# Performance work log

Hardware: AMD Instinct MI355X
Metric: run time of the kernel (lower is better)

The kernel has to match this reference:

```python
import jax, jax.numpy as jnp
import numpy as np

B, S, D = 2, 2048, 4096
H, KVH, HD = 32, 8, 128          # n_heads, n_kv_heads, head_dim
N_REP = H // KVH                 # GQA repeat factor
ROPE_THETA = 10000.0
NEG = -1e9                       # finite stand-in for -inf additive mask


def setup_inputs() -> dict:
    key = jax.random.key(0)
    ks = jax.random.split(key, 5)
    x = jax.random.normal(ks[0], (B, S, D), jnp.float32)
    wq = jax.random.normal(ks[1], (D, H * HD), jnp.float32) * 0.02
    wk = jax.random.normal(ks[2], (D, KVH * HD), jnp.float32) * 0.02
    wv = jax.random.normal(ks[3], (D, KVH * HD), jnp.float32) * 0.02
    wo = jax.random.normal(ks[4], (D, D), jnp.float32) * 0.02
    # rotary frequencies: freq_cis[t, j] = exp(i * t * theta^(-2j/HD))
    inv_freq = 1.0 / (ROPE_THETA ** (jnp.arange(0, HD, 2, dtype=jnp.float32) / HD))
    angles = jnp.arange(S, dtype=jnp.float32)[:, None] * inv_freq[None, :]  # [S, HD/2]
    cos, sin = jnp.cos(angles), jnp.sin(angles)
    # causal additive mask [S, S]
    i = jnp.arange(S)
    mask = jnp.where(i[None, :] > i[:, None], NEG, 0.0).astype(jnp.float32)
    return {"x": x, "cos": cos, "sin": sin, "mask": mask,
            "wq": wq, "wk": wk, "wv": wv, "wo": wo, "start_pos": 0}


def _apply_rope(t, cos, sin):
    # t: [B, S, nH, HD] -> rotate consecutive pairs, matching view_as_complex semantics
    tp = t.reshape(*t.shape[:-1], HD // 2, 2)
    t0, t1 = tp[..., 0], tp[..., 1]
    c = cos[None, :, None, :]  # [1, S, 1, HD/2]
    s = sin[None, :, None, :]
    o0 = t0 * c - t1 * s
    o1 = t0 * s + t1 * c
    return jnp.stack([o0, o1], axis=-1).reshape(t.shape)


def reference(x, cos, sin, mask, wq, wk, wv, wo, start_pos):
    bs, seq_len, _ = x.shape
    q = (x @ wq).reshape(bs, seq_len, H, HD)
    k = (x @ wk).reshape(bs, seq_len, KVH, HD)
    v = (x @ wv).reshape(bs, seq_len, KVH, HD)
    q = _apply_rope(q, cos, sin)
    k = _apply_rope(k, cos, sin)
    # start_pos == 0 full prefill: KV cache slice [:, :start_pos+seq_len] == k, v
    # GQA: repeat_interleave kv heads (each kv head repeated N_REP times consecutively)
    k = jnp.repeat(k, N_REP, axis=2)  # [B, S, H, HD]
    v = jnp.repeat(v, N_REP, axis=2)
    attn = jnp.einsum('bqhd,bkhd->bhqk', q, k) / jnp.sqrt(jnp.float32(HD))
    attn = attn + mask[None, None, :, :]
    p = jax.nn.softmax(attn.astype(jnp.float32), axis=-1).astype(q.dtype)
    out = jnp.einsum('bhqk,bkhd->bqhd', p, v).reshape(bs, seq_len, D)
    return out @ wo
```

## Files before the change

kernel.cpp:

```cpp
#include <hip/hip_runtime.h>
#include <stdint.h>

typedef unsigned short u16;
typedef __attribute__((ext_vector_type(8))) short bf16x8;
typedef __attribute__((ext_vector_type(4))) float f32x4;

#if __has_builtin(__builtin_amdgcn_exp2f)
  #define ATTN_EXP(x) __builtin_amdgcn_exp2f(x)
  #define ATTN_QSC 0.12751746f
  #define ATTN_NOFF -11.5415603f
#else
  #define ATTN_EXP(x) __expf(x)
  #define ATTN_QSC 0.08838834764831845f
  #define ATTN_NOFF -8.0f
#endif

__device__ __forceinline__ u16 f2bf(float f) {
  uint32_t x = __float_as_uint(f);
  x += 0x7fffu + ((x >> 16) & 1u);
  return (u16)(x >> 16);
}
__device__ __forceinline__ float bf2f(u16 u) {
  return __uint_as_float(((uint32_t)u) << 16);
}
__device__ __forceinline__ void gload_lds16(const void* g, void* l) {
  __builtin_amdgcn_global_load_lds(
      (const __attribute__((address_space(1))) void*)g,
      (__attribute__((address_space(3))) void*)l, 16, 0, 0);
}

__device__ __forceinline__ float rope_rot(float a, int col, int srow,
                                          const float* __restrict__ cosT,
                                          const float* __restrict__ sinT) {
  float p = __shfl_xor(a, 1, 64);
  int d = (col & 127) >> 1;
  float c = cosT[srow * 64 + d];
  float sn = sinT[srow * 64 + d];
  return (col & 1) ? (p * sn + a * c) : (a * c - p * sn);
}

__global__ __launch_bounds__(256) void cvt_kernel(const float* __restrict__ x,
                                                  u16* __restrict__ y) {
  int i = blockIdx.x * 256 + threadIdx.x;
  float4 v = ((const float4*)x)[i];
  ushort4 o = make_ushort4(f2bf(v.x), f2bf(v.y), f2bf(v.z), f2bf(v.w));
  ((ushort4*)y)[i] = o;
}

__global__ __launch_bounds__(256) void transpose_cvt(const float* __restrict__ W,
                                                     u16* __restrict__ Wt,
                                                     int Kd, int Nd) {
  __shared__ float t[32][33];
  int k0 = blockIdx.y * 32, n0 = blockIdx.x * 32;
  int tx = threadIdx.x, ty = threadIdx.y;
  #pragma unroll
  for (int i = ty; i < 32; i += 8)
    t[i][tx] = W[(size_t)(k0 + i) * Nd + n0 + tx];
  __syncthreads();
  #pragma unroll
  for (int i = ty; i < 32; i += 8)
    Wt[(size_t)(n0 + i) * Kd + k0 + tx] = f2bf(t[tx][i]);
}

__global__ __launch_bounds__(256, 2) void gemm_kv(const u16* __restrict__ A,
                                                  const u16* __restrict__ Bt,
                                                  u16* __restrict__ Kout,
                                                  u16* __restrict__ Vt,
                                                  const float* __restrict__ cosT,
                                                  const float* __restrict__ sinT) {
  const int K = 4096;
  const int NK = 64;
  __shared__ __attribute__((aligned(16))) u16 sA[3][128 * 64];
  __shared__ __attribute__((aligned(16))) u16 sB[2][128 * 64];
  const int tid = threadIdx.x;
  const int wave = tid >> 6, lane = tid & 63;
  const int lr = lane & 15, lq = lane >> 4;
  int lin = blockIdx.y * gridDim.x + blockIdx.x;
  int cpx = (gridDim.x * gridDim.y) >> 3;
  int swz = (lin & 7) * cpx + (lin >> 3);
  const int bm = (swz >> 4) * 128, bn = (swz & 15) * 128;
  const int wm = (wave >> 1) * 64, wn = (wave & 1) * 64;

  f32x4 acc[4][4] = {};

  auto stageA = [&](int j) {
    u16* dst = &sA[j % 3][0];
    #pragma unroll
    for (int c = 0; c < 4; ++c) {
      int e = (c * 256 + tid) * 8;
      int r = e >> 6, col = e & 63;
      gload_lds16(A + (size_t)(bm + r) * K + j * 64 + (col ^ ((r & 7) << 3)), dst + e);
    }
  };
  auto stageB = [&](int j) {
    u16* dst = &sB[j & 1][0];
    #pragma unroll
    for (int c = 0; c < 4; ++c) {
      int e = (c * 256 + tid) * 8;
      int r = e >> 6, col = e & 63;
      gload_lds16(Bt + (size_t)(bn + r) * K + j * 64 + (col ^ ((r & 7) << 3)), dst + e);
    }
  };
  auto readA = [&](bf16x8* af, const u16* a_, int ks) {
    #pragma unroll
    for (int mf = 0; mf < 4; ++mf) {
      int row = wm + mf * 16 + lr;
      af[mf] = *(const bf16x8*)(a_ + row * 64 + ((ks * 32 + lq * 8) ^ ((row & 7) << 3)));
    }
  };
  auto readB = [&](bf16x8* bfv, const u16* b_, int ks) {
    #pragma unroll
    for (int nf = 0; nf < 4; ++nf) {
      int row = wn + nf * 16 + lr;
      bfv[nf] = *(const bf16x8*)(b_ + row * 64 + ((ks * 32 + lq * 8) ^ ((row & 7) << 3)));
    }
  };

  bf16x8 afP[4], bfP[4], afQ[4], bfQ[4];

  stageA(0); stageB(0); stageA(1); stageB(1);
  asm volatile("s_waitcnt vmcnt(8)" ::: "memory");
  asm volatile("s_barrier" ::: "memory");
  readA(afP, sA[0], 0); readB(bfP, sB[0], 0);

  for (int j = 0; j < NK; ++j) {
    const u16* a_ = sA[j % 3];
    const u16* b_ = sB[j & 1];
    const u16* an = sA[(j + 1) % 3];
    const u16* bn_ = sB[(j + 1) & 1];
    readA(afQ, a_, 1); readB(bfQ, b_, 1);
    if (j + 2 < NK) stageA(j + 2);
    asm volatile("s_waitcnt lgkmcnt(8)" ::: "memory");
    __builtin_amdgcn_sched_barrier(0);
    __builtin_amdgcn_s_setprio(1);
    #pragma unroll
    for (int mf = 0; mf < 4; ++mf)
      #pragma unroll
      for (int nf = 0; nf < 4; ++nf)
        acc[mf][nf] = __builtin_amdgcn_mfma_f32_16x16x32_bf16(afP[mf], bfP[nf],
                                                              acc[mf][nf], 0, 0, 0);
    __builtin_amdgcn_s_setprio(0);
    if (j + 2 < NK) asm volatile("s_waitcnt vmcnt(4)" ::: "memory");
    else            asm volatile("s_waitcnt vmcnt(0)" ::: "memory");
    asm volatile("s_barrier" ::: "memory");
    readA(afP, an, 0); readB(bfP, bn_, 0);
    if (j + 2 < NK) stageB(j + 2);
    asm volatile("s_waitcnt lgkmcnt(8)" ::: "memory");
    __builtin_amdgcn_sched_barrier(0);
    __builtin_amdgcn_s_setprio(1);
    #pragma unroll
    for (int mf = 0; mf < 4; ++mf)
      #pragma unroll
      for (int nf = 0; nf < 4; ++nf)
        acc[mf][nf] = __builtin_amdgcn_mfma_f32_16x16x32_bf16(afQ[mf], bfQ[nf],
                                                              acc[mf][nf], 0, 0, 0);
    __builtin_amdgcn_s_setprio(0);
  }

  #pragma unroll
  for (int i = 0; i < 4; ++i) {
    #pragma unroll
    for (int j = 0; j < 4; ++j) {
      int colg = bn + wn + j * 16 + lr;
      if (bn < 1024) {
        #pragma unroll
        for (int r = 0; r < 4; ++r) {
          int row = bm + wm + i * 16 + lq * 4 + r;
          float o = rope_rot(acc[i][j][r], colg, row & 2047, cosT, sinT);
          Kout[(size_t)row * 1024 + colg] = f2bf(o);
        }
      } else {
        int col = colg - 1024;
        int row0 = bm + wm + i * 16 + lq * 4;
        int bb = row0 >> 11, s = row0 & 2047;
        ushort4 pk = make_ushort4(f2bf(acc[i][j][0]), f2bf(acc[i][j][1]),
                                  f2bf(acc[i][j][2]), f2bf(acc[i][j][3]));
        *(ushort4*)(Vt + ((size_t)bb * 1024 + col) * 2048 + s) = pk;
      }
    }
  }
}

template <int EPI, bool ROPE>
__global__ __launch_bounds__(512, 2) void gemm256(const u16* __restrict__ A,
                                                  const u16* __restrict__ Bt,
                                                  void* __restrict__ Cout,
                                                  int M, int N, int K,
                                                  const float* __restrict__ cosT,
                                                  const float* __restrict__ sinT,
                                                  float post) {
  __shared__ __attribute__((aligned(16))) u16 sA[3][256 * 64];
  __shared__ __attribute__((aligned(16))) u16 sB[2][256 * 64];
  const int tid = threadIdx.x;
  const int wid = tid >> 6, lane = tid & 63;
  const int lr = lane & 15, lq = lane >> 4;
  const int nbn = N >> 8;
  int lin = blockIdx.y * gridDim.x + blockIdx.x;
  int cpx = (gridDim.x * gridDim.y) >> 3;
  int swz = (lin & 7) * cpx + (lin >> 3);
  const int bm = (swz / nbn) * 256, bn = (swz % nbn) * 256;
  const int wrow = (wid >> 2) * 128, wcol = (wid & 3) * 64;
  const int NK = K >> 6;

  f32x4 acc[8][4] = {};

  auto stageA = [&](int j) {
    u16* dst = &sA[j % 3][0];
    #pragma unroll
    for (int c = 0; c < 4; ++c) {
      int e = (c * 512 + tid) * 8;
      int r = e >> 6, col = e & 63;
      gload_lds16(A + (size_t)(bm + r) * K + j * 64 + (col ^ ((r & 7) << 3)), dst + e);
    }
  };
  auto stageB = [&](int j) {
    u16* dst = &sB[j & 1][0];
    #pragma unroll
    for (int c = 0; c < 4; ++c) {
      int e = (c * 512 + tid) * 8;
      int r = e >> 6, col = e & 63;
      gload_lds16(Bt + (size_t)(bn + r) * K + j * 64 + (col ^ ((r & 7) << 3)), dst + e);
    }
  };
  auto readA = [&](bf16x8* af, const u16* a_, int ks) {
    #pragma unroll
    for (int mf = 0; mf < 8; ++mf) {
      int row = wrow + mf * 16 + lr;
      af[mf] = *(const bf16x8*)(a_ + row * 64 + ((ks * 32 + lq * 8) ^ ((row & 7) << 3)));
    }
  };
  auto readB = [&](bf16x8* bfv, const u16* b_, int ks) {
    #pragma unroll
    for (int nf = 0; nf < 4; ++nf) {
      int row = wcol + nf * 16 + lr;
      bfv[nf] = *(const bf16x8*)(b_ + row * 64 + ((ks * 32 + lq * 8) ^ ((row & 7) << 3)));
    }
  };

  bf16x8 afP[8], bfP[4], afQ[8], bfQ[4];

  stageB(0); stageA(0); stageA(1); stageB(1);
  asm volatile("s_waitcnt vmcnt(8)" ::: "memory");
  asm volatile("s_barrier" ::: "memory");
  readA(afP, sA[0], 0); readB(bfP, sB[0], 0);

  for (int j = 0; j < NK; ++j) {
    const u16* a_ = sA[j % 3];
    const u16* b_ = sB[j & 1];
    const u16* an = sA[(j + 1) % 3];
    const u16* bn = sB[(j + 1) & 1];
    readA(afQ, a_, 1); readB(bfQ, b_, 1);
    if (j + 2 < NK) stageA(j + 2);
    asm volatile("s_waitcnt lgkmcnt(12)" ::: "memory");
    __builtin_amdgcn_sched_barrier(0);
    __builtin_amdgcn_s_setprio(1);
    #pragma unroll
    for (int mf = 0; mf < 8; ++mf)
      #pragma unroll
      for (int nf = 0; nf < 4; ++nf)
        acc[mf][nf] = __builtin_amdgcn_mfma_f32_16x16x32_bf16(afP[mf], bfP[nf],
                                                              acc[mf][nf], 0, 0, 0);
    __builtin_amdgcn_s_setprio(0);
    if (j + 2 < NK) asm volatile("s_waitcnt vmcnt(4)" ::: "memory");
    else            asm volatile("s_waitcnt vmcnt(0)" ::: "memory");
    asm volatile("s_barrier" ::: "memory");
    readA(afP, an, 0); readB(bfP, bn, 0);
    if (j + 2 < NK) stageB(j + 2);
    asm volatile("s_waitcnt lgkmcnt(12)" ::: "memory");
    __builtin_amdgcn_sched_barrier(0);
    __builtin_amdgcn_s_setprio(1);
    #pragma unroll
    for (int mf = 0; mf < 8; ++mf)
      #pragma unroll
      for (int nf = 0; nf < 4; ++nf)
        acc[mf][nf] = __builtin_amdgcn_mfma_f32_16x16x32_bf16(afQ[mf], bfQ[nf],
                                                              acc[mf][nf], 0, 0, 0);
    __builtin_amdgcn_s_setprio(0);
  }

  #pragma unroll
  for (int mf = 0; mf < 8; ++mf) {
    #pragma unroll
    for (int nf = 0; nf < 4; ++nf) {
      #pragma unroll
      for (int r = 0; r < 4; ++r) {
        int row = bm + wrow + mf * 16 + lq * 4 + r;
        int col = bn + wcol + nf * 16 + lr;
        if (ROPE) {
          float o = rope_rot(acc[mf][nf][r], col, row & 2047, cosT, sinT);
          ((u16*)Cout)[(size_t)row * N + col] = f2bf(o * post);
        } else if (EPI == 0) {
          ((u16*)Cout)[(size_t)row * N + col] = f2bf(acc[mf][nf][r]);
        } else {
          ((float*)Cout)[(size_t)row * N + col] = acc[mf][nf][r];
        }
      }
    }
  }
}

__global__ __launch_bounds__(256, 2) void attn_kernel(const u16* __restrict__ Q,
                                                      const u16* __restrict__ Kb,
                                                      const u16* __restrict__ Vt,
                                                      u16* __restrict__ O) {
  __shared__ __attribute__((aligned(16))) u16 sK[2][64 * 128];
  __shared__ __attribute__((aligned(16))) u16 sV[2][128 * 64];
  __shared__ __attribute__((aligned(16))) u16 sP[4][16 * 64];
  const int tid = threadIdx.x;
  const int wave = tid >> 6, lane = tid & 63;
  const int lr = lane & 15, lq = lane >> 4;
  const int p = blockIdx.x & 15;
  const int h = (blockIdx.x >> 4) & 31;
  const int b = blockIdx.x >> 9;
  const int kvh = h >> 2;
  const int qtA = p, qtB = 31 - p;
  const int q0A = qtA * 64 + wave * 16;
  const int q0B = qtB * 64 + wave * 16;
  const float NOFF = ATTN_NOFF;

  bf16x8 qfA[4], qfB[4];
  {
    const u16* qa = Q + (size_t)(b * 2048 + q0A + lr) * 4096 + h * 128 + lq * 8;
    const u16* qb = Q + (size_t)(b * 2048 + q0B + lr) * 4096 + h * 128 + lq * 8;
    #pragma unroll
    for (int ks = 0; ks < 4; ++ks) {
      qfA[ks] = *(const bf16x8*)(qa + ks * 32);
      qfB[ks] = *(const bf16x8*)(qb + ks * 32);
    }
  }

  const u16* kbase = Kb + (size_t)b * 2048 * 1024 + kvh * 128;
  const u16* vbase = Vt + (size_t)(b * 1024 + kvh * 128) * 2048;

  auto stage = [&](int kt, int bsel) {
    #pragma unroll
    for (int c = 0; c < 4; ++c) {
      int chunk = wave * 4 + c;
      int eo = chunk * 512 + lane * 8;
      int rk = eo >> 7, ck = eo & 127;
      int cks = ck ^ ((rk & 7) << 3);
      gload_lds16(kbase + (size_t)(kt * 64 + rk) * 1024 + cks,
                  (u16*)sK[bsel] + chunk * 512);
      int rv = eo >> 6, cv = eo & 63;
      int cvs = cv ^ ((rv & 7) << 3);
      gload_lds16(vbase + (size_t)rv * 2048 + kt * 64 + cvs,
                  (u16*)sV[bsel] + chunk * 512);
    }
  };

  f32x4 oA[8] = {}, oB[8] = {};
  float lA = 0.f, lB = 0.f;

  stage(0, 0);
  __syncthreads();
  int buf = 0;
  for (int kt = 0; kt <= qtB; ++kt) {
    if (kt < qtB) stage(kt + 1, buf ^ 1);
    const u16* kb_ = sK[buf];
    const u16* vb_ = sV[buf];
    const bool doA = (kt <= qtA);

    f32x4 sAacc[4], sBacc[4];
    #pragma unroll
    for (int nf = 0; nf < 4; ++nf) {
      sAacc[nf] = (f32x4){NOFF, NOFF, NOFF, NOFF};
      sBacc[nf] = (f32x4){NOFF, NOFF, NOFF, NOFF};
    }
    __builtin_amdgcn_s_setprio(1);
    #pragma unroll
    for (int ks = 0; ks < 4; ++ks) {
      bf16x8 kf[4];
      #pragma unroll
      for (int nf = 0; nf < 4; ++nf) {
        int row = nf * 16 + lr;
        kf[nf] = *(const bf16x8*)(kb_ + row * 128 + ((ks * 32 + lq * 8) ^ ((row & 7) << 3)));
      }
      #pragma unroll
      for (int nf = 0; nf < 4; ++nf)
        sBacc[nf] = __builtin_amdgcn_mfma_f32_16x16x32_bf16(kf[nf], qfB[ks], sBacc[nf], 0, 0, 0);
      if (doA) {
        #pragma unroll
        for (int nf = 0; nf < 4; ++nf)
          sAacc[nf] = __builtin_amdgcn_mfma_f32_16x16x32_bf16(kf[nf], qfA[ks], sAacc[nf], 0, 0, 0);
      }
    }
    __builtin_amdgcn_s_setprio(0);

    auto sm_pv = [&](f32x4* sacc, float& lsum, f32x4* o, int qt, int q0) {
      float ls = 0.f;
      const bool diag = (kt == qt);
      #pragma unroll
      for (int nf = 0; nf < 4; ++nf) {
        float pv0, pv1, pv2, pv3;
        {
          float v0 = ATTN_EXP(sacc[nf][0]);
          float v1 = ATTN_EXP(sacc[nf][1]);
          float v2 = ATTN_EXP(sacc[nf][2]);
          float v3 = ATTN_EXP(sacc[nf][3]);
          if (diag) {
            int kbase_ = kt * 64 + nf * 16 + lq * 4;
            int q = q0 + lr;
            if (kbase_ + 0 > q) v0 = 0.f;
            if (kbase_ + 1 > q) v1 = 0.f;
            if (kbase_ + 2 > q) v2 = 0.f;
            if (kbase_ + 3 > q) v3 = 0.f;
          }
          pv0 = v0; pv1 = v1; pv2 = v2; pv3 = v3;
        }
        ls += (pv0 + pv1) + (pv2 + pv3);
        uint32_t p01, p23;
        asm("v_cvt_pk_bf16_f32 %0, %1, %2" : "=v"(p01) : "v"(pv0), "v"(pv1));
        asm("v_cvt_pk_bf16_f32 %0, %1, %2" : "=v"(p23) : "v"(pv2), "v"(pv3));
        uint32_t* dst = (uint32_t*)((char*)sP[wave] +
                          ((lr * 128 + nf * 32 + lq * 8) ^ ((lr & 7) << 4)));
        dst[0] = p01;
        dst[1] = p23;
      }
      lsum += ls;
      __builtin_amdgcn_s_setprio(1);
      #pragma unroll
      for (int ks = 0; ks < 2; ++ks) {
        bf16x8 pa = *(const bf16x8*)((const char*)sP[wave] +
                        ((lr * 128 + ks * 64 + lq * 16) ^ ((lr & 7) << 4)));
        #pragma unroll
        for (int df = 0; df < 8; ++df) {
          int row = df * 16 + lr;
          bf16x8 vb = *(const bf16x8*)(vb_ + row * 64 + ((ks * 32 + lq * 8) ^ ((row & 7) << 3)));
          o[df] = __builtin_amdgcn_mfma_f32_16x16x32_bf16(pa, vb, o[df], 0, 0, 0);
        }
      }
      __builtin_amdgcn_s_setprio(0);
    };

    if (doA) sm_pv(sAacc, lA, oA, qtA, q0A);
    sm_pv(sBacc, lB, oB, qtB, q0B);

    __syncthreads();
    buf ^= 1;
  }

  float tA = lA, tB = lB;
  tA += __shfl_xor(tA, 16, 64); tB += __shfl_xor(tB, 16, 64);
  tA += __shfl_xor(tA, 32, 64); tB += __shfl_xor(tB, 32, 64);
  tA = 1.f / tA; tB = 1.f / tB;
  float liA[4], liB[4];
  #pragma unroll
  for (int r = 0; r < 4; ++r) {
    liA[r] = __shfl(tA, lq * 4 + r, 64);
    liB[r] = __shfl(tB, lq * 4 + r, 64);
  }
  #pragma unroll
  for (int df = 0; df < 8; ++df) {
    #pragma unroll
    for (int r = 0; r < 4; ++r) {
      int iqA = q0A + lq * 4 + r;
      int iqB = q0B + lq * 4 + r;
      O[(size_t)(b * 2048 + iqA) * 4096 + h * 128 + df * 16 + lr] = f2bf(oA[df][r] * liA[r]);
      O[(size_t)(b * 2048 + iqB) * 4096 + h * 128 + df * 16 + lr] = f2bf(oB[df][r] * liB[r]);
    }
  }
}

extern "C" void kernel_launch(void* const* d_in, const int* in_sizes, int n_in,
                              void* d_out, int out_size, void* d_ws, size_t ws_size,
                              hipStream_t stream) {
  (void)in_sizes; (void)n_in; (void)out_size;
  const float* x    = (const float*)d_in[0];
  const float* cosT = (const float*)d_in[1];
  const float* sinT = (const float*)d_in[2];
  const float* wq   = (const float*)d_in[4];
  const float* wk   = (const float*)d_in[5];
  const float* wv   = (const float*)d_in[6];
  const float* wo   = (const float*)d_in[7];
  float* out = (float*)d_out;
  char* ws = (char*)d_ws;

  const size_t WS_NEEDED = 201326592;
  if (ws_size < WS_NEEDED) return;

  u16* xb   = (u16*)(ws);
  u16* wqt  = (u16*)(ws + 33554432ULL);
  u16* wkvt = (u16*)(ws + 67108864ULL);
  u16* wot  = (u16*)(ws + 83886080ULL);
  u16* Qb   = (u16*)(ws + 117440512ULL);
  u16* Kbf  = (u16*)(ws + 150994944ULL);
  u16* Vt   = (u16*)(ws + 159383552ULL);
  u16* Ob   = (u16*)(ws + 167772160ULL);

  const float QSC = ATTN_QSC;

  cvt_kernel<<<16384, 256, 0, stream>>>(x, xb);
  transpose_cvt<<<dim3(128, 128), dim3(32, 8), 0, stream>>>(wq, wqt, 4096, 4096);
  transpose_cvt<<<dim3(32, 128),  dim3(32, 8), 0, stream>>>(wk, wkvt, 4096, 1024);
  transpose_cvt<<<dim3(32, 128),  dim3(32, 8), 0, stream>>>(wv, wkvt + 1024ULL * 4096, 4096, 1024);
  transpose_cvt<<<dim3(128, 128), dim3(32, 8), 0, stream>>>(wo, wot, 4096, 4096);

  gemm256<0, true><<<dim3(16, 16), 512, 0, stream>>>(xb, wqt, Qb, 4096, 4096, 4096,
                                                     cosT, sinT, QSC);
  gemm_kv<<<dim3(16, 32), 256, 0, stream>>>(xb, wkvt, Kbf, Vt, cosT, sinT);

  attn_kernel<<<1024, 256, 0, stream>>>(Qb, Kbf, Vt, Ob);

  gemm256<2, false><<<dim3(16, 16), 512, 0, stream>>>(Ob, wot, out, 4096, 4096, 4096,
                                                      nullptr, nullptr, 1.0f);
}
```

Measured before the change: 490.6 us.

## Process two GQA heads per attention block sharing staged K/V tiles

```diff
diff --git a/kernel.cpp b/kernel.cpp
--- a/kernel.cpp
+++ b/kernel.cpp
@@ -299,23 +299,26 @@
   }
 }
 
-__global__ __launch_bounds__(256, 2) void attn_kernel(const u16* __restrict__ Q,
+__global__ __launch_bounds__(512, 2) void attn_kernel(const u16* __restrict__ Q,
                                                       const u16* __restrict__ Kb,
                                                       const u16* __restrict__ Vt,
                                                       u16* __restrict__ O) {
   __shared__ __attribute__((aligned(16))) u16 sK[2][64 * 128];
   __shared__ __attribute__((aligned(16))) u16 sV[2][128 * 64];
-  __shared__ __attribute__((aligned(16))) u16 sP[4][16 * 64];
+  __shared__ __attribute__((aligned(16))) u16 sP[8][16 * 64];
   const int tid = threadIdx.x;
   const int wave = tid >> 6, lane = tid & 63;
   const int lr = lane & 15, lq = lane >> 4;
+  const int w4 = wave & 3;
+  const int hl = wave >> 2;
   const int p = blockIdx.x & 15;
-  const int h = (blockIdx.x >> 4) & 31;
-  const int b = blockIdx.x >> 9;
-  const int kvh = h >> 2;
+  const int hp = (blockIdx.x >> 4) & 1;
+  const int kvh = (blockIdx.x >> 5) & 7;
+  const int b = blockIdx.x >> 8;
+  const int h = kvh * 4 + hp * 2 + hl;
   const int qtA = p, qtB = 31 - p;
-  const int q0A = qtA * 64 + wave * 16;
-  const int q0B = qtB * 64 + wave * 16;
+  const int q0A = qtA * 64 + w4 * 16;
+  const int q0B = qtB * 64 + w4 * 16;
   const float NOFF = ATTN_NOFF;
 
   bf16x8 qfA[4], qfB[4];
@@ -334,8 +337,8 @@
 
   auto stage = [&](int kt, int bsel) {
     #pragma unroll
-    for (int c = 0; c < 4; ++c) {
-      int chunk = wave * 4 + c;
+    for (int c = 0; c < 2; ++c) {
+      int chunk = wave * 2 + c;
       int eo = chunk * 512 + lane * 8;
       int rk = eo >> 7, ck = eo & 127;
       int cks = ck ^ ((rk & 7) << 3);
@@ -391,26 +394,22 @@
       const bool diag = (kt == qt);
       #pragma unroll
       for (int nf = 0; nf < 4; ++nf) {
-        float pv0, pv1, pv2, pv3;
-        {
-          float v0 = ATTN_EXP(sacc[nf][0]);
-          float v1 = ATTN_EXP(sacc[nf][1]);
-          float v2 = ATTN_EXP(sacc[nf][2]);
-          float v3 = ATTN_EXP(sacc[nf][3]);
-          if (diag) {
-            int kbase_ = kt * 64 + nf * 16 + lq * 4;
-            int q = q0 + lr;
-            if (kbase_ + 0 > q) v0 = 0.f;
-            if (kbase_ + 1 > q) v1 = 0.f;
-            if (kbase_ + 2 > q) v2 = 0.f;
-            if (kbase_ + 3 > q) v3 = 0.f;
-          }
-          pv0 = v0; pv1 = v1; pv2 = v2; pv3 = v3;
+        float v0 = ATTN_EXP(sacc[nf][0]);
+        float v1 = ATTN_EXP(sacc[nf][1]);
+        float v2 = ATTN_EXP(sacc[nf][2]);
+        float v3 = ATTN_EXP(sacc[nf][3]);
+        if (diag) {
+          int kb0 = kt * 64 + nf * 16 + lq * 4;
+          int q = q0 + lr;
+          if (kb0 + 0 > q) v0 = 0.f;
+          if (kb0 + 1 > q) v1 = 0.f;
+          if (kb0 + 2 > q) v2 = 0.f;
+          if (kb0 + 3 > q) v3 = 0.f;
         }
-        ls += (pv0 + pv1) + (pv2 + pv3);
+        ls += (v0 + v1) + (v2 + v3);
         uint32_t p01, p23;
-        asm("v_cvt_pk_bf16_f32 %0, %1, %2" : "=v"(p01) : "v"(pv0), "v"(pv1));
-        asm("v_cvt_pk_bf16_f32 %0, %1, %2" : "=v"(p23) : "v"(pv2), "v"(pv3));
+        asm("v_cvt_pk_bf16_f32 %0, %1, %2" : "=v"(p01) : "v"(v0), "v"(v1));
+        asm("v_cvt_pk_bf16_f32 %0, %1, %2" : "=v"(p23) : "v"(v2), "v"(v3));
         uint32_t* dst = (uint32_t*)((char*)sP[wave] +
                           ((lr * 128 + nf * 32 + lq * 8) ^ ((lr & 7) << 4)));
         dst[0] = p01;
@@ -499,7 +498,7 @@
                                                      cosT, sinT, QSC);
   gemm_kv<<<dim3(16, 32), 256, 0, stream>>>(xb, wkvt, Kbf, Vt, cosT, sinT);
 
-  attn_kernel<<<1024, 256, 0, stream>>>(Qb, Kbf, Vt, Ob);
+  attn_kernel<<<512, 512, 0, stream>>>(Qb, Kbf, Vt, Ob);
 
   gemm256<2, false><<<dim3(16, 16), 512, 0, stream>>>(Ob, wot, out, 4096, 4096, 4096,
                                                       nullptr, nullptr, 1.0f);
```

Result: no change. 494.6 us (+0.8%).
